# Kernel optimization log

Measured on AMD Instinct MI355X. Metric: run time of the kernel, lower is better.

## Reference

```python
import jax, jax.numpy as jnp
import numpy as np
import math

BOUND = 1e-06
PI = math.pi

N_DIMS = 256
N_ROWS = 524288
DELTA = 1e-06


def _make_buffers(n_dims, delta, radius, scaling, range_type="bound"):
    if range_type == "whole":
        phi_L = 0.0
    else:  # 'bound'
        L = 0.01
        upper_bound = PI / 2 * (1.0 - L)
        phi_L = math.asin(delta ** (1.0 / n_dims))
        phi_L = phi_L if phi_L < upper_bound else upper_bound
    # W_theta: identity with last row duplicated -> (n_dims+1, n_dims)
    eye = np.eye(n_dims, dtype=np.float32)
    W_theta = np.concatenate([eye, eye[-1:]], axis=0)
    # W_phi: strictly upper-triangular ones, with [-2, -1] zeroed
    W_phi = np.triu(np.ones((n_dims + 1, n_dims + 1), dtype=np.float32), k=1)
    W_phi[-2, -1] = 0.0
    b_phi = np.zeros(n_dims + 1, dtype=np.float32)
    b_phi[-1] = -PI / 2.0
    return (
        jnp.float32(phi_L),
        jnp.asarray(W_theta),
        jnp.asarray(W_phi),
        jnp.asarray(b_phi),
        jnp.float32(radius),
        jnp.float32(scaling),
    )


def setup_inputs() -> dict:
    key = jax.random.key(0)
    x = jax.random.normal(key, (N_ROWS, N_DIMS), dtype=jnp.float32)
    phi_L, W_theta, W_phi, b_phi, radius, scaling = _make_buffers(
        N_DIMS, DELTA, radius=1.0, scaling=1.0, range_type="bound"
    )
    return {
        "x": x,
        "W_theta": W_theta,
        "W_phi": W_phi,
        "b_phi": b_phi,
        "phi_L": phi_L,
        "radius": radius,
        "scaling": scaling,
    }


def reference(x, W_theta, W_phi, b_phi, phi_L, radius, scaling):
    # Map features to angles in [phi_L, pi/2)
    ang = (PI / 2 - phi_L) * jax.nn.sigmoid(scaling * x) + phi_L
    # Duplicate last angle: [N, n_dims] -> [N, n_dims+1]
    a = jnp.matmul(ang, W_theta.T)
    # log-sin cumulative sum (via strictly-upper-triangular matmul) + log-cos term
    logx = jnp.matmul(jnp.log(jnp.sin(a) + BOUND), W_phi) + jnp.log(
        jnp.cos(a + b_phi) + BOUND
    )
    return radius * jnp.exp(logx)
```

## Files before the change

kernel.cpp:

```cpp
#include <hip/hip_runtime.h>

#define BOUND 1e-6f
#define HALF_PI 1.57079632679489662f
#define LOG2E 1.44269504088896341f

typedef float f32x4 __attribute__((ext_vector_type(4)));

#define UPD_DPP(oldv, srcv, ctrl, rmask)                                        \
  __int_as_float(__builtin_amdgcn_update_dpp(                                   \
      __float_as_int(oldv), __float_as_int(srcv), (ctrl), (rmask), 0xF, false))

__device__ __forceinline__ float wave_incl_prod(float x) {
    x *= UPD_DPP(1.0f, x, 0x111, 0xF);
    x *= UPD_DPP(1.0f, x, 0x112, 0xF);
    x *= UPD_DPP(1.0f, x, 0x114, 0xF);
    x *= UPD_DPP(1.0f, x, 0x118, 0xF);
    x *= UPD_DPP(1.0f, x, 0x142, 0xA);
    x *= UPD_DPP(1.0f, x, 0x143, 0xC);
    return x;
}

__global__ __launch_bounds__(256) void spherize_kernel(
    const float* __restrict__ x,
    const float* __restrict__ p_phiL,
    const float* __restrict__ p_radius,
    const float* __restrict__ p_scaling,
    float* __restrict__ out,
    int n_rows)
{
    __shared__ float lds[16 * 257];

    const float phi_L  = p_phiL[0];
    const float radius = p_radius[0];
    const float cexp   = p_scaling[0] * LOG2E;
    const float amp    = HALF_PI - phi_L;

    const int tid  = threadIdx.x;
    const int lane = tid & 63;
    const int wave = tid >> 6;
    const int row0 = blockIdx.x * 16;
    const int wrow = row0 + wave * 4;

    const int nr_blk = min(16, n_rows - row0);
    const int nr_w   = min(4, max(0, n_rows - wrow));

    f32x4 xv[4];
    const f32x4* xb =
        reinterpret_cast<const f32x4*>(x + (size_t)wrow * 256 + lane * 4);
    #pragma unroll
    for (int i = 0; i < 4; ++i)
        if (i < nr_w) xv[i] = __builtin_nontemporal_load(xb + i * 64);

    #pragma unroll
    for (int i = 0; i < 4; ++i) {
        if (i >= nr_w) break;
        float s[4], c[4];
        #pragma unroll
        for (int k = 0; k < 4; ++k) {
            float e  = __builtin_amdgcn_exp2f(cexp * xv[i][k]);
            float u  = amp * __builtin_amdgcn_rcpf(1.0f + e);
            float u2 = u * u;
            s[k] = fmaf(u2, fmaf(u2, 4.16666667e-2f, -0.5f), 1.0f + BOUND);
            float p = fmaf(u2, fmaf(u2, 8.33333333e-3f, -1.66666667e-1f), 1.0f);
            c[k] = fmaf(u, p, BOUND);
        }

        float q1 = s[0];
        float q2 = q1 * s[1];
        float q3 = q2 * s[2];
        float t  = q3 * s[3];
        float scan = wave_incl_prod(t);
        float excl = UPD_DPP(1.0f, scan, 0x138, 0xF);
        float base = radius * excl;

        float* lrow = lds + (wave * 4 + i) * 257 + lane * 4;
        lrow[0] = base * c[0];
        lrow[1] = base * q1 * c[1];
        lrow[2] = base * q2 * c[2];
        lrow[3] = base * q3 * c[3];
        if (lane == 63)
            lrow[4] = radius * scan;
    }
    __syncthreads();

    float* obase = out + (size_t)row0 * 257;
    if (nr_blk == 16) {
        const f32x4* l4 = reinterpret_cast<const f32x4*>(lds);
        f32x4*       o4 = reinterpret_cast<f32x4*>(obase);
        __builtin_nontemporal_store(l4[tid],       o4 + tid);
        __builtin_nontemporal_store(l4[tid + 256], o4 + tid + 256);
        __builtin_nontemporal_store(l4[tid + 512], o4 + tid + 512);
        __builtin_nontemporal_store(l4[tid + 768], o4 + tid + 768);
        if (tid < 4)
            __builtin_nontemporal_store(l4[tid + 1024], o4 + tid + 1024);
    } else {
        const int nd = nr_blk * 257;
        for (int i = tid; i < nd; i += 256) obase[i] = lds[i];
    }
}

extern "C" void kernel_launch(void* const* d_in, const int* in_sizes, int n_in,
                              void* d_out, int out_size, void* d_ws, size_t ws_size,
                              hipStream_t stream) {
    const float* x         = (const float*)d_in[0];
    const float* p_phiL    = (const float*)d_in[4];
    const float* p_radius  = (const float*)d_in[5];
    const float* p_scaling = (const float*)d_in[6];
    float* out = (float*)d_out;

    const int n_rows = in_sizes[0] / 256;
    const int blocks = (n_rows + 15) / 16;

    spherize_kernel<<<blocks, 256, 0, stream>>>(x, p_phiL, p_radius, p_scaling,
                                                out, n_rows);
}
```

Measured before the change: 186.8 us.

## Use single-wave blocks processing 16 rows to remove block barrier

Each block is now one 64-lane wave that loads, computes and stores all 16 rows itself. The __syncthreads barrier is replaced by a wave-local LDS waitcnt, and the write-out loop iterates per lane. This is meant to remove cross-wave barrier stalls and increase per-wave memory parallelism. In exchange, each wave holds 16 vector loads in registers, and LDS per block stays the same, so fewer waves per CU may be resident.

```diff
diff --git a/kernel.cpp b/kernel.cpp
--- a/kernel.cpp
+++ b/kernel.cpp
@@ -20,7 +20,7 @@
     return x;
 }
 
-__global__ __launch_bounds__(256) void spherize_kernel(
+__global__ __launch_bounds__(64) void spherize_kernel(
     const float* __restrict__ x,
     const float* __restrict__ p_phiL,
     const float* __restrict__ p_radius,
@@ -35,25 +35,20 @@
     const float cexp   = p_scaling[0] * LOG2E;
     const float amp    = HALF_PI - phi_L;
 
-    const int tid  = threadIdx.x;
-    const int lane = tid & 63;
-    const int wave = tid >> 6;
+    const int lane = threadIdx.x & 63;
     const int row0 = blockIdx.x * 16;
-    const int wrow = row0 + wave * 4;
+    const int nr   = min(16, n_rows - row0);
 
-    const int nr_blk = min(16, n_rows - row0);
-    const int nr_w   = min(4, max(0, n_rows - wrow));
-
-    f32x4 xv[4];
+    f32x4 xv[16];
     const f32x4* xb =
-        reinterpret_cast<const f32x4*>(x + (size_t)wrow * 256 + lane * 4);
+        reinterpret_cast<const f32x4*>(x + (size_t)row0 * 256 + lane * 4);
     #pragma unroll
-    for (int i = 0; i < 4; ++i)
-        if (i < nr_w) xv[i] = __builtin_nontemporal_load(xb + i * 64);
+    for (int i = 0; i < 16; ++i)
+        if (i < nr) xv[i] = __builtin_nontemporal_load(xb + i * 64);
 
     #pragma unroll
-    for (int i = 0; i < 4; ++i) {
-        if (i >= nr_w) break;
+    for (int i = 0; i < 16; ++i) {
+        if (i >= nr) break;
         float s[4], c[4];
         #pragma unroll
         for (int k = 0; k < 4; ++k) {
@@ -73,7 +68,7 @@
         float excl = UPD_DPP(1.0f, scan, 0x138, 0xF);
         float base = radius * excl;
 
-        float* lrow = lds + (wave * 4 + i) * 257 + lane * 4;
+        float* lrow = lds + i * 257 + lane * 4;
         lrow[0] = base * c[0];
         lrow[1] = base * q1 * c[1];
         lrow[2] = base * q2 * c[2];
@@ -81,21 +76,21 @@
         if (lane == 63)
             lrow[4] = radius * scan;
     }
-    __syncthreads();
+
+    asm volatile("s_waitcnt lgkmcnt(0)" ::: "memory");
 
     float* obase = out + (size_t)row0 * 257;
-    if (nr_blk == 16) {
+    if (nr == 16) {
         const f32x4* l4 = reinterpret_cast<const f32x4*>(lds);
         f32x4*       o4 = reinterpret_cast<f32x4*>(obase);
-        __builtin_nontemporal_store(l4[tid],       o4 + tid);
-        __builtin_nontemporal_store(l4[tid + 256], o4 + tid + 256);
-        __builtin_nontemporal_store(l4[tid + 512], o4 + tid + 512);
-        __builtin_nontemporal_store(l4[tid + 768], o4 + tid + 768);
-        if (tid < 4)
-            __builtin_nontemporal_store(l4[tid + 1024], o4 + tid + 1024);
+        #pragma unroll
+        for (int j = 0; j < 16; ++j)
+            __builtin_nontemporal_store(l4[j * 64 + lane], o4 + j * 64 + lane);
+        if (lane < 4)
+            __builtin_nontemporal_store(l4[1024 + lane], o4 + 1024 + lane);
     } else {
-        const int nd = nr_blk * 257;
-        for (int i = tid; i < nd; i += 256) obase[i] = lds[i];
+        const int nd = nr * 257;
+        for (int i = lane; i < nd; i += 64) obase[i] = lds[i];
     }
 }
 
@@ -111,6 +106,6 @@
     const int n_rows = in_sizes[0] / 256;
     const int blocks = (n_rows + 15) / 16;
 
-    spherize_kernel<<<blocks, 256, 0, stream>>>(x, p_phiL, p_radius, p_scaling,
-                                                out, n_rows);
+    spherize_kernel<<<blocks, 64, 0, stream>>>(x, p_phiL, p_radius, p_scaling,
+                                               out, n_rows);
 }
```

New measurement: 432.0 us. 2.31x slower.
